# Performance work log

Measured on AMD Instinct MI355X. Metric: run time of the kernel, lower is better.

Reference implementation:

```python
import jax, jax.numpy as jnp
import numpy as np

SEQ, B, XD = 2048, 4, 16
D, NH, DFF, L, M = 256, 8, 512, 2, 1024
DH = D // NH
NEG_INF = -1e9  # finite stand-in for -inf (same softmax result, grad-safe)


def setup_inputs() -> dict:
    key = jax.random.key(0)
    ks = iter(jax.random.split(key, 40))

    def w(shape, s=0.02):
        return jax.random.normal(next(ks), shape, dtype=jnp.float32) * s

    return {
        "x": jax.random.normal(next(ks), (SEQ, B, XD), dtype=jnp.float32),
        "y": jax.random.normal(next(ks), (SEQ, B), dtype=jnp.float32),
        "single_eval_pos": M,
        "xenc_w": w((D, XD)), "xenc_b": w((D,)),
        "yenc_w": w((D, 1)), "yenc_b": w((D,)),
        "in_proj_w": w((L, 3 * D, D)), "in_proj_b": w((L, 3 * D)),
        "out_proj_w": w((L, D, D)), "out_proj_b": w((L, D)),
        "ln1_g": jnp.ones((L, D), jnp.float32), "ln1_b": jnp.zeros((L, D), jnp.float32),
        "lin1_w": w((L, DFF, D)), "lin1_b": w((L, DFF)),
        "lin2_w": w((L, D, DFF)), "lin2_b": w((L, D)),
        "ln2_g": jnp.ones((L, D), jnp.float32), "ln2_b": jnp.zeros((L, D), jnp.float32),
        "head_w1": w((DFF, D)), "head_b1": w((DFF,)),
        "head_w2": w((1, DFF)), "head_b2": w((1,)),
    }


def _layer_norm(x, g, b, eps=1e-5):
    mu = jnp.mean(x, axis=-1, keepdims=True)
    var = jnp.var(x, axis=-1, keepdims=True)
    return (x - mu) * jax.lax.rsqrt(var + eps) * g + b


def _forward(x, y, M_, p):
    seq, batch = y.shape
    x_src = x @ p["xenc_w"].T + p["xenc_b"]                     # [seq, b, D]
    y_src = y[..., None] @ p["yenc_w"].T + p["yenc_b"]           # [seq, b, D]
    tokens = jnp.concatenate([x_src[:M_] + y_src[:M_], x_src[M_:]], axis=0)

    # prefix-block + diagonal mask: keep (j < M) or (i == j)
    i = jnp.arange(seq)
    keep = (i[None, :] < M_) | (i[:, None] == i[None, :])
    mask = jnp.where(keep, 0.0, NEG_INF).astype(tokens.dtype)    # [seq, seq]

    h = tokens
    for l in range(p["in_proj_w"].shape[0]):
        qkv = h @ p["in_proj_w"][l].T + p["in_proj_b"][l]        # [seq, b, 3D]
        q, k, v = jnp.split(qkv, 3, axis=-1)
        to_heads = lambda t: t.reshape(seq, batch, NH, DH).transpose(1, 2, 0, 3)
        q, k, v = to_heads(q), to_heads(k), to_heads(v)          # [b, h, s, dh]
        scores = jnp.einsum("bhqd,bhkd->bhqk", q, k) / np.float32(np.sqrt(DH)) + mask
        attn = jax.nn.softmax(scores, axis=-1)
        o = jnp.einsum("bhqk,bhkd->bhqd", attn, v)
        o = o.transpose(2, 0, 1, 3).reshape(seq, batch, D)
        o = o @ p["out_proj_w"][l].T + p["out_proj_b"][l]
        h = _layer_norm(h + o, p["ln1_g"][l], p["ln1_b"][l])      # post-norm
        ff = jax.nn.gelu(h @ p["lin1_w"][l].T + p["lin1_b"][l], approximate=False)
        ff = ff @ p["lin2_w"][l].T + p["lin2_b"][l]
        h = _layer_norm(h + ff, p["ln2_g"][l], p["ln2_b"][l])

    q_out = h[M_:]                                               # [seq-M, b, D]
    hid = jax.nn.gelu(q_out @ p["head_w1"].T + p["head_b1"], approximate=False)
    return hid @ p["head_w2"].T + p["head_b2"]                   # [seq-M, b, 1]


def reference(x, y, single_eval_pos, xenc_w, xenc_b, yenc_w, yenc_b,
              in_proj_w, in_proj_b, out_proj_w, out_proj_b,
              ln1_g, ln1_b, lin1_w, lin1_b, lin2_w, lin2_b, ln2_g, ln2_b,
              head_w1, head_b1, head_w2, head_b2):
    p = dict(xenc_w=xenc_w, xenc_b=xenc_b, yenc_w=yenc_w, yenc_b=yenc_b,
             in_proj_w=in_proj_w, in_proj_b=in_proj_b,
             out_proj_w=out_proj_w, out_proj_b=out_proj_b,
             ln1_g=ln1_g, ln1_b=ln1_b, lin1_w=lin1_w, lin1_b=lin1_b,
             lin2_w=lin2_w, lin2_b=lin2_b, ln2_g=ln2_g, ln2_b=ln2_b,
             head_w1=head_w1, head_b1=head_b1, head_w2=head_w2, head_b2=head_b2)
    return _forward(x, y, int(single_eval_pos), p)
```

## Files before the change

### kernel.cpp

```cpp
#include <hip/hip_runtime.h>
#include <hip/hip_bf16.h>
#include <math.h>

#define SEQ    2048
#define BATCH  4
#define XDIM   16
#define DMODEL 256
#define NHEAD  8
#define DH     32
#define DFF    512
#define NLAYER 2
#define MPOS   1024
#define ROWS   (SEQ*BATCH)

#define ATT_SCALE 0.17677669529663687f
#define BK 32

typedef __attribute__((ext_vector_type(8))) short bf16x8;
typedef __attribute__((ext_vector_type(4))) float f32x4;

__device__ __forceinline__ float gelu_exact(float x) {
    return 0.5f * x * (1.0f + erff(x * 0.70710678118654752f));
}
__device__ __forceinline__ short f2bf(float f) {
    unsigned int u = __float_as_uint(f);
    u += 0x7FFFu + ((u >> 16) & 1u);
    return (short)(u >> 16);
}
__device__ __forceinline__ float bf2f(unsigned short u) {
    return __uint_as_float(((unsigned int)u) << 16);
}
__device__ __forceinline__ void gload16(const unsigned short* g, unsigned short* l) {
    __builtin_amdgcn_global_load_lds(
        (const __attribute__((address_space(1))) unsigned int*)g,
        (__attribute__((address_space(3))) unsigned int*)l, 16, 0, 0);
}
#define VMWAIT(N) asm volatile("s_waitcnt vmcnt(" #N ")" ::: "memory")
__device__ __forceinline__ void pipe_barrier() {
    __builtin_amdgcn_sched_barrier(0);
    __builtin_amdgcn_s_barrier();
    __builtin_amdgcn_sched_barrier(0);
}

__global__ __launch_bounds__(256) void encode_cast(
    const float* __restrict__ x, const float* __restrict__ y,
    const float* __restrict__ xw, const float* __restrict__ xb,
    const float* __restrict__ yw, const float* __restrict__ yb,
    float* __restrict__ h, unsigned short* __restrict__ hb,
    const float* __restrict__ s0, const float* __restrict__ s1,
    const float* __restrict__ s2, const float* __restrict__ s3,
    const float* __restrict__ s4,
    unsigned short* __restrict__ d0, unsigned short* __restrict__ d1,
    unsigned short* __restrict__ d2, unsigned short* __restrict__ d3,
    unsigned short* __restrict__ d4)
{
    if (blockIdx.x < ROWS/4) {
        int g = blockIdx.x;
        int d = threadIdx.x;
        __shared__ float xs[4][XDIM];
        __shared__ float ys[4];
        if (d < 64) xs[d>>4][d&15] = x[(size_t)(g*4 + (d>>4))*XDIM + (d&15)];
        if (d < 4)  ys[d] = y[g*4 + d];
        __syncthreads();
        float wreg[XDIM];
        #pragma unroll
        for (int k = 0; k < XDIM; ++k) wreg[k] = xw[d*XDIM + k];
        const float xbv = xb[d], ywv = yw[d], ybv = yb[d];
        const bool train = (g < MPOS);
        #pragma unroll
        for (int r = 0; r < 4; ++r) {
            int row = g*4 + r;
            float acc = xbv;
            #pragma unroll
            for (int k = 0; k < XDIM; ++k) acc = fmaf(xs[r][k], wreg[k], acc);
            if (train) acc += ys[r]*ywv + ybv;
            h[(size_t)row*DMODEL + d]  = acc;
            hb[(size_t)row*DMODEL + d] = (unsigned short)f2bf(acc);
        }
        return;
    }
    int i = (blockIdx.x - ROWS/4)*256 + threadIdx.x;
    if (i >= 147456) return;
    const float* s; unsigned short* d; int off;
    if      (i <  49152) { s = s0; d = d0; off = i; }
    else if (i <  65536) { s = s1; d = d1; off = i - 49152; }
    else if (i <  98304) { s = s2; d = d2; off = i - 65536; }
    else if (i < 131072) { s = s3; d = d3; off = i - 98304; }
    else                 { s = s4; d = d4; off = i - 131072; }
    float4 a = *(const float4*)(s + (size_t)off*8);
    float4 c = *(const float4*)(s + (size_t)off*8 + 4);
    ushort4 u0, u1;
    u0.x=(unsigned short)f2bf(a.x); u0.y=(unsigned short)f2bf(a.y);
    u0.z=(unsigned short)f2bf(a.z); u0.w=(unsigned short)f2bf(a.w);
    u1.x=(unsigned short)f2bf(c.x); u1.y=(unsigned short)f2bf(c.y);
    u1.z=(unsigned short)f2bf(c.z); u1.w=(unsigned short)f2bf(c.w);
    *(ushort4*)(d + (size_t)off*8)     = u0;
    *(ushort4*)(d + (size_t)off*8 + 4) = u1;
}

__global__ __launch_bounds__(256) void gemm_qkv(
    const unsigned short* __restrict__ A, const unsigned short* __restrict__ B,
    const float* __restrict__ bias,
    unsigned short* __restrict__ Qg, unsigned short* __restrict__ Kg,
    unsigned short* __restrict__ Vg, int K)
{
    __shared__ unsigned short As[3][128][BK];
    __shared__ unsigned short Bs[3][64][BK];
    int tid  = threadIdx.x;
    int w    = tid >> 6, lane = tid & 63;
    int col  = lane & 15, quad = lane >> 4;
    int u    = blockIdx.x >> 3, xcd = blockIdx.x & 7;
    int by   = xcd*8 + u/12, bx = u%12;
    int m0   = by * 128, n0 = bx * 64;
    int l4   = lane >> 2, c8 = (lane & 3) * 8;

    f32x4 acc[2][4];
    #pragma unroll
    for (int i = 0; i < 2; ++i)
        #pragma unroll
        for (int j = 0; j < 4; ++j) acc[i][j] = (f32x4){0.f,0.f,0.f,0.f};

    const unsigned short* ga = A + (size_t)(m0 + w*32 + l4)*K + c8;
    const unsigned short* gb = B + (size_t)(n0 + w*16 + l4)*K + c8;

    const int NS = K / BK;
    gload16(ga,                  &As[0][w*32     ][0]);
    gload16(ga + (size_t)16*K,   &As[0][w*32 + 16][0]);
    gload16(gb,                  &Bs[0][w*16     ][0]);
    gload16(ga + BK,                  &As[1][w*32     ][0]);
    gload16(ga + BK + (size_t)16*K,   &As[1][w*32 + 16][0]);
    gload16(gb + BK,                  &Bs[1][w*16     ][0]);

    int bcur = 0;
    for (int s = 0; s < NS; ++s) {
        if (s == NS - 1) { VMWAIT(0); } else { VMWAIT(3); }
        pipe_barrier();
        if (s + 2 < NS) {
            int bpre = bcur + 2; if (bpre >= 3) bpre -= 3;
            int k2 = (s + 2) * BK;
            gload16(ga + k2,                &As[bpre][w*32     ][0]);
            gload16(ga + k2 + (size_t)16*K, &As[bpre][w*32 + 16][0]);
            gload16(gb + k2,                &Bs[bpre][w*16     ][0]);
        }
        bf16x8 af[2], bfr[4];
        #pragma unroll
        for (int i = 0; i < 2; ++i) af[i]  = *(const bf16x8*)&As[bcur][w*32 + i*16 + col][quad*8];
        #pragma unroll
        for (int j = 0; j < 4; ++j) bfr[j] = *(const bf16x8*)&Bs[bcur][j*16 + col][quad*8];
        #pragma unroll
        for (int i = 0; i < 2; ++i)
            #pragma unroll
            for (int j = 0; j < 4; ++j)
                acc[i][j] = __builtin_amdgcn_mfma_f32_16x16x32_bf16(bfr[j], af[i], acc[i][j], 0, 0, 0);
        bcur = (bcur == 2) ? 0 : bcur + 1;
    }

    int region = n0 >> 8;
    if (region < 2) {
        #pragma unroll
        for (int i = 0; i < 2; ++i) {
            int m = m0 + w*32 + i*16 + col;
            int s = m >> 2, bidx = m & 3;
            #pragma unroll
            for (int j = 0; j < 4; ++j) {
                int ng = n0 + j*16 + quad*4;
                float4 bi = *(const float4*)&bias[ng];
                ushort4 uu;
                uu.x=(unsigned short)f2bf(acc[i][j][0] + bi.x);
                uu.y=(unsigned short)f2bf(acc[i][j][1] + bi.y);
                uu.z=(unsigned short)f2bf(acc[i][j][2] + bi.z);
                uu.w=(unsigned short)f2bf(acc[i][j][3] + bi.w);
                int np = ng - (region << 8);
                int hh = np >> 5, d = np & 31;
                int bh = bidx*NHEAD + hh;
                if (region == 0)
                    *(ushort4*)(Qg + ((size_t)(bh*SEQ + s))*DH + d) = uu;
                else
                    *(ushort4*)(Kg + ((size_t)(bh*SEQ + s))*DH + d) = uu;
            }
        }
    } else {
        __syncthreads();
        unsigned short* T3 = (unsigned short*)As;
        #pragma unroll
        for (int i = 0; i < 2; ++i) {
            int mi = w*32 + i*16 + col;
            int ss = mi >> 2, bidx = mi & 3;
            #pragma unroll
            for (int j = 0; j < 4; ++j) {
                int ni = j*16 + quad*4;
                float4 bi = *(const float4*)&bias[n0 + ni];
                T3[((ni    )*4 + bidx)*32 + ss] = (unsigned short)f2bf(acc[i][j][0] + bi.x);
                T3[((ni + 1)*4 + bidx)*32 + ss] = (unsigned short)f2bf(acc[i][j][1] + bi.y);
                T3[((ni + 2)*4 + bidx)*32 + ss] = (unsigned short)f2bf(acc[i][j][2] + bi.z);
                T3[((ni + 3)*4 + bidx)*32 + ss] = (unsigned short)f2bf(acc[i][j][3] + bi.w);
            }
        }
        __syncthreads();
        int sBase = m0 >> 2;
        #pragma unroll
        for (int r = 0; r < 4; ++r) {
            int chunk = tid + 256*r;
            int l = chunk >> 2, p = chunk & 3;
            int d = l & 31, hh_l = (l >> 5) & 1, bidx = l >> 6;
            int ni = hh_l*32 + d;
            int hh = ((n0 & 255) + ni) >> 5;
            int bh = bidx*NHEAD + hh;
            uint4 val = *(const uint4*)&T3[(ni*4 + bidx)*32 + p*8];
            *(uint4*)(Vg + ((size_t)(bh*DH + d))*SEQ + sBase + p*8) = val;
        }
    }
}

__global__ __launch_bounds__(256) void attn_mfma(
    const unsigned short* __restrict__ Qg,
    const unsigned short* __restrict__ Kg,
    const unsigned short* __restrict__ Vg,
    unsigned short* __restrict__ o)
{
    const int id  = blockIdx.x;
    const int sl  = id >> 3;
    const int bh  = (id & 7) * 4 + (sl >> 4);
    const int qt2 = sl & 15;
    const int h   = bh & 7;
    const int b   = bh >> 3;
    const int q0A = qt2 * 64;
    const int q0B = MPOS + qt2 * 64;
    const int tid  = threadIdx.x;
    const int w    = tid >> 6;
    const int lane = tid & 63;
    const int col  = lane & 15;
    const int quad = lane >> 4;

    __shared__ unsigned short Kt[2][64][40];
    __shared__ unsigned short Vt[2][32][72];
    __shared__ unsigned short PtA[4][16][72];
    __shared__ unsigned short PtB[4][16][72];

    const int qA = q0A + 16*w + col;
    const int qB = q0B + 16*w + col;
    bf16x8 qfA = *(const bf16x8*)(Qg + ((size_t)(bh*SEQ + qA))*DH + quad*8);
    bf16x8 qfB = *(const bf16x8*)(Qg + ((size_t)(bh*SEQ + qB))*DH + quad*8);

    f32x4 O0A = {0.f,0.f,0.f,0.f}, O1A = {0.f,0.f,0.f,0.f};
    f32x4 O0B = {0.f,0.f,0.f,0.f}, O1B = {0.f,0.f,0.f,0.f};
    float lsumA = 0.f, lsumB = 0.f;

    const int kRow = tid >> 2, kCh = (tid & 3) * 8;
    const int vD   = tid >> 3, vCh = (tid & 7) * 8;

    uint4 kreg = *(const uint4*)(Kg + ((size_t)(bh*SEQ + kRow))*DH + kCh);
    uint4 vreg = *(const uint4*)(Vg + ((size_t)(bh*DH + vD))*SEQ + vCh);

    for (int kt = 0; kt < 17; ++kt) {
        const bool self = (kt == 16);
        const int  p    = kt & 1;
        *(uint4*)&Kt[p][kRow][kCh] = kreg;
        *(uint4*)&Vt[p][vD][vCh]   = vreg;
        __syncthreads();
        if (kt < 16) {
            int kn = (kt == 15) ? q0B : (kt + 1)*64;
            kreg = *(const uint4*)(Kg + ((size_t)(bh*SEQ + kn + kRow))*DH + kCh);
            vreg = *(const uint4*)(Vg + ((size_t)(bh*DH + vD))*SEQ + kn + vCh);
        }

        #pragma unroll
        for (int mt = 0; mt < 4; ++mt) {
            bf16x8 kf = *(const bf16x8*)&Kt[p][mt*16 + col][quad*8];
            if (!self) {
                f32x4 stA = {0.f,0.f,0.f,0.f};
                stA = __builtin_amdgcn_mfma_f32_16x16x32_bf16(kf, qfA, stA, 0, 0, 0);
                ushort4 pwA;
                #pragma unroll
                for (int i = 0; i < 4; ++i) {
                    float pv = __expf(stA[i]*ATT_SCALE);
                    unsigned short us = (unsigned short)f2bf(pv);
                    ((unsigned short*)&pwA)[i] = us;
                    lsumA += bf2f(us);
                }
                *(ushort4*)&PtA[w][col][mt*16 + quad*4] = pwA;
            }
            f32x4 stB = {0.f,0.f,0.f,0.f};
            stB = __builtin_amdgcn_mfma_f32_16x16x32_bf16(kf, qfB, stB, 0, 0, 0);
            ushort4 pwB;
            #pragma unroll
            for (int i = 0; i < 4; ++i) {
                float pv = __expf(stB[i]*ATT_SCALE);
                if (self && (mt*16 + quad*4 + i != 16*w + col)) pv = 0.f;
                unsigned short us = (unsigned short)f2bf(pv);
                ((unsigned short*)&pwB)[i] = us;
                lsumB += bf2f(us);
            }
            *(ushort4*)&PtB[w][col][mt*16 + quad*4] = pwB;
        }
        #pragma unroll
        for (int c = 0; c < 2; ++c) {
            bf16x8 v0 = *(const bf16x8*)&Vt[p][col     ][c*32 + quad*8];
            bf16x8 v1 = *(const bf16x8*)&Vt[p][col + 16][c*32 + quad*8];
            if (!self) {
                bf16x8 pfA = *(const bf16x8*)&PtA[w][col][c*32 + quad*8];
                O0A = __builtin_amdgcn_mfma_f32_16x16x32_bf16(v0, pfA, O0A, 0, 0, 0);
                O1A = __builtin_amdgcn_mfma_f32_16x16x32_bf16(v1, pfA, O1A, 0, 0, 0);
            }
            bf16x8 pfB = *(const bf16x8*)&PtB[w][col][c*32 + quad*8];
            O0B = __builtin_amdgcn_mfma_f32_16x16x32_bf16(v0, pfB, O0B, 0, 0, 0);
            O1B = __builtin_amdgcn_mfma_f32_16x16x32_bf16(v1, pfB, O1B, 0, 0, 0);
        }
    }

    lsumA += __shfl_xor(lsumA, 16, 64); lsumA += __shfl_xor(lsumA, 32, 64);
    lsumB += __shfl_xor(lsumB, 16, 64); lsumB += __shfl_xor(lsumB, 32, 64);
    float invA = 1.0f / lsumA, invB = 1.0f / lsumB;
    ushort4 u0, u1;
    #pragma unroll
    for (int i = 0; i < 4; ++i) {
        ((unsigned short*)&u0)[i] = (unsigned short)f2bf(O0A[i]*invA);
        ((unsigned short*)&u1)[i] = (unsigned short)f2bf(O1A[i]*invA);
    }
    unsigned short* opA = o + ((size_t)(qA*BATCH + b))*DMODEL + h*DH;
    *(ushort4*)(opA + quad*4)      = u0;
    *(ushort4*)(opA + 16 + quad*4) = u1;
    #pragma unroll
    for (int i = 0; i < 4; ++i) {
        ((unsigned short*)&u0)[i] = (unsigned short)f2bf(O0B[i]*invB);
        ((unsigned short*)&u1)[i] = (unsigned short)f2bf(O1B[i]*invB);
    }
    unsigned short* opB = o + ((size_t)(qB*BATCH + b))*DMODEL + h*DH;
    *(ushort4*)(opB + quad*4)      = u0;
    *(ushort4*)(opB + 16 + quad*4) = u1;
}

__global__ __launch_bounds__(256) void mlp_fused(
    const unsigned short* __restrict__ attb,
    const unsigned short* __restrict__ Wout, const float* __restrict__ ob,
    const float* __restrict__ g1, const float* __restrict__ be1,
    const unsigned short* __restrict__ W1, const float* __restrict__ fb1,
    const unsigned short* __restrict__ W2, const float* __restrict__ fb2,
    const float* __restrict__ g2, const float* __restrict__ be2,
    float* __restrict__ h, unsigned short* __restrict__ hb,
    const unsigned short* __restrict__ Wh1, const float* __restrict__ hb1,
    const float* __restrict__ hw2, const float* __restrict__ hb2,
    float* __restrict__ out, int doHead)
{
    __shared__ unsigned short Bs[3][256][64];
    __shared__ __align__(16) unsigned char smem_u[33280];
    __shared__ unsigned short Ht[2][16][264];
    __shared__ float sP[2][4][16], qP[2][4][16];

    typedef unsigned short AsT[2][16][64];
    AsT* As = reinterpret_cast<AsT*>(smem_u);
    typedef unsigned short PtT[16][520];
    PtT* Pt = reinterpret_cast<PtT*>(smem_u);

    const int tid  = threadIdx.x;
    const int w    = tid >> 6;
    const int lane = tid & 63;
    const int col  = lane & 15;
    const int quad = lane >> 4;
    const int l8   = lane >> 3;
    const int c8s  = (((lane & 7) ^ l8) * 8);
    const int bid  = blockIdx.x;
    const int m0a  = bid * 16;
    const int m0b  = 4096 + bid * 16;
    const int ma   = m0a + col;
    const int mb   = m0b + col;

    float resid[2][4][4];

    {
        f32x4 acc[2][4];
        #pragma unroll
        for (int g = 0; g < 2; ++g)
            #pragma unroll
            for (int j = 0; j < 4; ++j) acc[g][j] = (f32x4){0.f,0.f,0.f,0.f};

        const int gr = w >> 1;
        const unsigned short* gaw = attb + (size_t)((gr ? m0b : m0a) + (w&1)*8 + l8)*DMODEL + c8s;
        const unsigned short* gb  = Wout + (size_t)(w*64 + l8)*DMODEL + c8s;
        const int NS = DMODEL / 64;

        #pragma unroll
        for (int pb = 0; pb < 2; ++pb) {
            int k = pb * 64;
            gload16(gaw + k, &As[pb][gr][(w&1)*8][0]);
            #pragma unroll
            for (int t = 0; t < 8; ++t)
                gload16(gb + k + (size_t)(t*8)*DMODEL, &Bs[pb][w*64 + t*8][0]);
        }
        int bcur = 0;
        for (int s = 0; s < NS; ++s) {
            if (s == NS - 1) { VMWAIT(0); } else { VMWAIT(9); }
            pipe_barrier();
            if (s + 2 < NS) {
                int bpre = bcur + 2; if (bpre >= 3) bpre -= 3;
                int k2 = (s + 2) * 64;
                gload16(gaw + k2, &As[bpre][gr][(w&1)*8][0]);
                #pragma unroll
                for (int t = 0; t < 8; ++t)
                    gload16(gb + k2 + (size_t)(t*8)*DMODEL, &Bs[bpre][w*64 + t*8][0]);
            }
            #pragma unroll
            for (int kk = 0; kk < 2; ++kk) {
                const int so = (((kk*4 + quad) ^ (col & 7)) * 8);
                bf16x8 af0 = *(const bf16x8*)&As[bcur][0][col][so];
                bf16x8 af1 = *(const bf16x8*)&As[bcur][1][col][so];
                #pragma unroll
                for (int j = 0; j < 4; ++j) {
                    bf16x8 bfr = *(const bf16x8*)&Bs[bcur][w*64 + j*16 + col][so];
                    acc[0][j] = __builtin_amdgcn_mfma_f32_16x16x32_bf16(bfr, af0, acc[0][j], 0, 0, 0);
                    acc[1][j] = __builtin_amdgcn_mfma_f32_16x16x32_bf16(bfr, af1, acc[1][j], 0, 0, 0);
                }
            }
            bcur = (bcur == 2) ? 0 : bcur + 1;
        }

        float ssum[2] = {0.f, 0.f}, qsum[2] = {0.f, 0.f};
        #pragma unroll
        for (int g = 0; g < 2; ++g) {
            int m = g ? mb : ma;
            #pragma unroll
            for (int j = 0; j < 4; ++j) {
                int n = w*64 + j*16 + quad*4;
                float4 bi = *(const float4*)&ob[n];
                float4 hv = *(const float4*)&h[(size_t)m*DMODEL + n];
                #pragma unroll
                for (int i = 0; i < 4; ++i) {
                    float val = acc[g][j][i] + ((const float*)&bi)[i] + ((const float*)&hv)[i];
                    resid[g][j][i] = val;
                    ssum[g] += val; qsum[g] += val*val;
                }
            }
        }
        #pragma unroll
        for (int g = 0; g < 2; ++g) {
            ssum[g] += __shfl_xor(ssum[g], 16, 64); ssum[g] += __shfl_xor(ssum[g], 32, 64);
            qsum[g] += __shfl_xor(qsum[g], 16, 64); qsum[g] += __shfl_xor(qsum[g], 32, 64);
        }
        if (quad == 0) {
            sP[0][w][col] = ssum[0]; qP[0][w][col] = qsum[0];
            sP[1][w][col] = ssum[1]; qP[1][w][col] = qsum[1];
        }
        __syncthreads();
        #pragma unroll
        for (int g = 0; g < 2; ++g) {
            float st = sP[g][0][col] + sP[g][1][col] + sP[g][2][col] + sP[g][3][col];
            float qt = qP[g][0][col] + qP[g][1][col] + qP[g][2][col] + qP[g][3][col];
            float mu   = st * (1.0f/DMODEL);
            float var  = qt * (1.0f/DMODEL) - mu*mu;
            float rstd = rsqrtf(var + 1e-5f);
            #pragma unroll
            for (int j = 0; j < 4; ++j) {
                int n = w*64 + j*16 + quad*4;
                float4 gv = *(const float4*)&g1[n];
                float4 bv = *(const float4*)&be1[n];
                ushort4 u;
                #pragma unroll
                for (int i = 0; i < 4; ++i) {
                    float o = (resid[g][j][i]-mu)*rstd*((const float*)&gv)[i] + ((const float*)&bv)[i];
                    resid[g][j][i] = o;
                    ((unsigned short*)&u)[i] = (unsigned short)f2bf(o);
                }
                *(ushort4*)&Ht[g][col][n] = u;
            }
        }
        __syncthreads();
    }

    #pragma unroll 1
    for (int nh = 0; nh < 2; ++nh) {
        f32x4 acc[2][4];
        #pragma unroll
        for (int g = 0; g < 2; ++g)
            #pragma unroll
            for (int j = 0; j < 4; ++j) acc[g][j] = (f32x4){0.f,0.f,0.f,0.f};
        const unsigned short* gb = W1 + (size_t)(nh*256 + w*64 + l8)*DMODEL + c8s;
        const int NS = DMODEL / 64;

        #pragma unroll
        for (int pb = 0; pb < 2; ++pb)
            #pragma unroll
            for (int t = 0; t < 8; ++t)
                gload16(gb + pb*64 + (size_t)(t*8)*DMODEL, &Bs[pb][w*64 + t*8][0]);

        int bcur = 0;
        for (int s = 0; s < NS; ++s) {
            if (s == NS - 1) { VMWAIT(0); } else { VMWAIT(8); }
            pipe_barrier();
            if (s + 2 < NS) {
                int bpre = bcur + 2; if (bpre >= 3) bpre -= 3;
                int k2 = (s + 2) * 64;
                #pragma unroll
                for (int t = 0; t < 8; ++t)
                    gload16(gb + k2 + (size_t)(t*8)*DMODEL, &Bs[bpre][w*64 + t*8][0]);
            }
            #pragma unroll
            for (int kk = 0; kk < 2; ++kk) {
                const int so = (((kk*4 + quad) ^ (col & 7)) * 8);
                bf16x8 af0 = *(const bf16x8*)&Ht[0][col][s*64 + kk*32 + quad*8];
                bf16x8 af1 = *(const bf16x8*)&Ht[1][col][s*64 + kk*32 + quad*8];
                #pragma unroll
                for (int j = 0; j < 4; ++j) {
                    bf16x8 bfr = *(const bf16x8*)&Bs[bcur][w*64 + j*16 + col][so];
                    acc[0][j] = __builtin_amdgcn_mfma_f32_16x16x32_bf16(bfr, af0, acc[0][j], 0, 0, 0);
                    acc[1][j] = __builtin_amdgcn_mfma_f32_16x16x32_bf16(bfr, af1, acc[1][j], 0, 0, 0);
                }
            }
            bcur = (bcur == 2) ? 0 : bcur + 1;
        }
        #pragma unroll
        for (int g = 0; g < 2; ++g)
            #pragma unroll
            for (int j = 0; j < 4; ++j) {
                int n2 = nh*256 + w*64 + j*16 + quad*4;
                float4 bi = *(const float4*)&fb1[n2];
                ushort4 u;
                #pragma unroll
                for (int i = 0; i < 4; ++i)
                    ((unsigned short*)&u)[i] = (unsigned short)f2bf(gelu_exact(acc[g][j][i] + ((const float*)&bi)[i]));
                *(ushort4*)&Pt[g][col][n2] = u;
            }
        pipe_barrier();
    }

    {
        __syncthreads();
        f32x4 acc[2][4];
        #pragma unroll
        for (int g = 0; g < 2; ++g)
            #pragma unroll
            for (int j = 0; j < 4; ++j) acc[g][j] = (f32x4){0.f,0.f,0.f,0.f};
        const unsigned short* gb = W2 + (size_t)(w*64 + l8)*DFF + c8s;
        const int NS = DFF / 64;

        #pragma unroll
        for (int pb = 0; pb < 2; ++pb)
            #pragma unroll
            for (int t = 0; t < 8; ++t)
                gload16(gb + pb*64 + (size_t)(t*8)*DFF, &Bs[pb][w*64 + t*8][0]);

        int bcur = 0;
        for (int s = 0; s < NS; ++s) {
            if (s == NS - 1) { VMWAIT(0); } else { VMWAIT(8); }
            pipe_barrier();
            if (s + 2 < NS) {
                int bpre = bcur + 2; if (bpre >= 3) bpre -= 3;
                int k2 = (s + 2) * 64;
                #pragma unroll
                for (int t = 0; t < 8; ++t)
                    gload16(gb + k2 + (size_t)(t*8)*DFF, &Bs[bpre][w*64 + t*8][0]);
            }
            #pragma unroll
            for (int kk = 0; kk < 2; ++kk) {
                const int so = (((kk*4 + quad) ^ (col & 7)) * 8);
                bf16x8 af0 = *(const bf16x8*)&Pt[0][col][s*64 + kk*32 + quad*8];
                bf16x8 af1 = *(const bf16x8*)&Pt[1][col][s*64 + kk*32 + quad*8];
                #pragma unroll
                for (int j = 0; j < 4; ++j) {
                    bf16x8 bfr = *(const bf16x8*)&Bs[bcur][w*64 + j*16 + col][so];
                    acc[0][j] = __builtin_amdgcn_mfma_f32_16x16x32_bf16(bfr, af0, acc[0][j], 0, 0, 0);
                    acc[1][j] = __builtin_amdgcn_mfma_f32_16x16x32_bf16(bfr, af1, acc[1][j], 0, 0, 0);
                }
            }
            bcur = (bcur == 2) ? 0 : bcur + 1;
        }

        float ssum[2] = {0.f, 0.f}, qsum[2] = {0.f, 0.f};
        #pragma unroll
        for (int g = 0; g < 2; ++g)
            #pragma unroll
            for (int j = 0; j < 4; ++j) {
                int n = w*64 + j*16 + quad*4;
                float4 bi = *(const float4*)&fb2[n];
                #pragma unroll
                for (int i = 0; i < 4; ++i) {
                    float val = acc[g][j][i] + ((const float*)&bi)[i] + resid[g][j][i];
                    resid[g][j][i] = val;
                    ssum[g] += val; qsum[g] += val*val;
                }
            }
        #pragma unroll
        for (int g = 0; g < 2; ++g) {
            ssum[g] += __shfl_xor(ssum[g], 16, 64); ssum[g] += __shfl_xor(ssum[g], 32, 64);
            qsum[g] += __shfl_xor(qsum[g], 16, 64); qsum[g] += __shfl_xor(qsum[g], 32, 64);
        }
        if (quad == 0) {
            sP[0][w][col] = ssum[0]; qP[0][w][col] = qsum[0];
            sP[1][w][col] = ssum[1]; qP[1][w][col] = qsum[1];
        }
        __syncthreads();
        #pragma unroll
        for (int g = 0; g < 2; ++g) {
            int m = g ? mb : ma;
            float st = sP[g][0][col] + sP[g][1][col] + sP[g][2][col] + sP[g][3][col];
            float qt = qP[g][0][col] + qP[g][1][col] + qP[g][2][col] + qP[g][3][col];
            float mu   = st * (1.0f/DMODEL);
            float var  = qt * (1.0f/DMODEL) - mu*mu;
            float rstd = rsqrtf(var + 1e-5f);
            #pragma unroll
            for (int j = 0; j < 4; ++j) {
                int n = w*64 + j*16 + quad*4;
                float4 gv = *(const float4*)&g2[n];
                float4 bv = *(const float4*)&be2[n];
                float4 o;
                ushort4 u;
                #pragma unroll
                for (int i = 0; i < 4; ++i) {
                    float ov = (resid[g][j][i]-mu)*rstd*((const float*)&gv)[i] + ((const float*)&bv)[i];
                    ((float*)&o)[i] = ov;
                    ((unsigned short*)&u)[i] = (unsigned short)f2bf(ov);
                }
                *(float4*)&h[(size_t)m*DMODEL + n] = o;
                *(ushort4*)(hb + (size_t)m*DMODEL + n) = u;
                *(ushort4*)&Ht[g][col][n] = u;
            }
        }
        __syncthreads();
    }

    if (doHead) {
        float sdot = 0.f;
        #pragma unroll 1
        for (int nh = 0; nh < 2; ++nh) {
            f32x4 acc[4];
            #pragma unroll
            for (int j = 0; j < 4; ++j) acc[j] = (f32x4){0.f,0.f,0.f,0.f};
            const unsigned short* gb = Wh1 + (size_t)(nh*256 + w*64 + l8)*DMODEL + c8s;
            const int NS = DMODEL / 64;

            #pragma unroll
            for (int pb = 0; pb < 2; ++pb)
                #pragma unroll
                for (int t = 0; t < 8; ++t)
                    gload16(gb + pb*64 + (size_t)(t*8)*DMODEL, &Bs[pb][w*64 + t*8][0]);

            int bcur = 0;
            for (int s = 0; s < NS; ++s) {
                if (s == NS - 1) { VMWAIT(0); } else { VMWAIT(8); }
                pipe_barrier();
                if (s + 2 < NS) {
                    int bpre = bcur + 2; if (bpre >= 3) bpre -= 3;
                    int k2 = (s + 2) * 64;
                    #pragma unroll
                    for (int t = 0; t < 8; ++t)
                        gload16(gb + k2 + (size_t)(t*8)*DMODEL, &Bs[bpre][w*64 + t*8][0]);
                }
                #pragma unroll
                for (int kk = 0; kk < 2; ++kk) {
                    const int so = (((kk*4 + quad) ^ (col & 7)) * 8);
                    bf16x8 af = *(const bf16x8*)&Ht[1][col][s*64 + kk*32 + quad*8];
                    #pragma unroll
                    for (int j = 0; j < 4; ++j) {
                        bf16x8 bfr = *(const bf16x8*)&Bs[bcur][w*64 + j*16 + col][so];
                        acc[j] = __builtin_amdgcn_mfma_f32_16x16x32_bf16(bfr, af, acc[j], 0, 0, 0);
                    }
                }
                bcur = (bcur == 2) ? 0 : bcur + 1;
            }
            #pragma unroll
            for (int j = 0; j < 4; ++j) {
                int n2 = nh*256 + w*64 + j*16 + quad*4;
                float4 b1v = *(const float4*)&hb1[n2];
                float4 w2v = *(const float4*)&hw2[n2];
                #pragma unroll
                for (int i = 0; i < 4; ++i)
                    sdot += gelu_exact(acc[j][i] + ((const float*)&b1v)[i]) * ((const float*)&w2v)[i];
            }
            pipe_barrier();
        }
        sdot += __shfl_xor(sdot, 16, 64); sdot += __shfl_xor(sdot, 32, 64);
        if (quad == 0) sP[0][w][col] = sdot;
        __syncthreads();
        if (tid < 16)
            out[bid*16 + tid] = sP[0][0][tid] + sP[0][1][tid] + sP[0][2][tid] + sP[0][3][tid] + hb2[0];
    }
}

extern "C" void kernel_launch(void* const* d_in, const int* in_sizes, int n_in,
                              void* d_out, int out_size, void* d_ws, size_t ws_size,
                              hipStream_t stream)
{
    const float* x        = (const float*)d_in[0];
    const float* y        = (const float*)d_in[1];
    const float* xenc_w   = (const float*)d_in[3];
    const float* xenc_b   = (const float*)d_in[4];
    const float* yenc_w   = (const float*)d_in[5];
    const float* yenc_b   = (const float*)d_in[6];
    const float* in_proj_w  = (const float*)d_in[7];
    const float* in_proj_b  = (const float*)d_in[8];
    const float* out_proj_w = (const float*)d_in[9];
    const float* out_proj_b = (const float*)d_in[10];
    const float* ln1_g    = (const float*)d_in[11];
    const float* ln1_b    = (const float*)d_in[12];
    const float* lin1_w   = (const float*)d_in[13];
    const float* lin1_b   = (const float*)d_in[14];
    const float* lin2_w   = (const float*)d_in[15];
    const float* lin2_b   = (const float*)d_in[16];
    const float* ln2_g    = (const float*)d_in[17];
    const float* ln2_b    = (const float*)d_in[18];
    const float* head_w1  = (const float*)d_in[19];
    const float* head_b1  = (const float*)d_in[20];
    const float* head_w2  = (const float*)d_in[21];
    const float* head_b2  = (const float*)d_in[22];
    float* out = (float*)d_out;

    float* ws  = (float*)d_ws;
    float* h    = ws;
    unsigned short* hb    = (unsigned short*)(h + (size_t)ROWS*DMODEL);
    unsigned short* attb  = hb    + (size_t)ROWS*DMODEL;
    unsigned short* Qg    = attb  + (size_t)ROWS*DMODEL;
    unsigned short* Kg    = Qg    + (size_t)BATCH*NHEAD*SEQ*DH;
    unsigned short* Vg    = Kg    + (size_t)BATCH*NHEAD*SEQ*DH;
    unsigned short* Wqkv  = Vg    + (size_t)BATCH*NHEAD*SEQ*DH;
    unsigned short* Wout  = Wqkv  + (size_t)NLAYER*3*DMODEL*DMODEL;
    unsigned short* Wl1   = Wout  + (size_t)NLAYER*DMODEL*DMODEL;
    unsigned short* Wl2   = Wl1   + (size_t)NLAYER*DFF*DMODEL;
    unsigned short* Wh1   = Wl2   + (size_t)NLAYER*DMODEL*DFF;

    encode_cast<<<ROWS/4 + 576, 256, 0, stream>>>(
        x, y, xenc_w, xenc_b, yenc_w, yenc_b, h, hb,
        in_proj_w, out_proj_w, lin1_w, lin2_w, head_w1,
        Wqkv, Wout, Wl1, Wl2, Wh1);

    for (int l = 0; l < NLAYER; ++l) {
        gemm_qkv<<<768, 256, 0, stream>>>(
            hb, Wqkv + (size_t)l*3*DMODEL*DMODEL, in_proj_b + l*3*DMODEL,
            Qg, Kg, Vg, DMODEL);
        attn_mfma<<<512, 256, 0, stream>>>(Qg, Kg, Vg, attb);
        mlp_fused<<<256, 256, 0, stream>>>(
            attb,
            Wout + (size_t)l*DMODEL*DMODEL, out_proj_b + l*DMODEL,
            ln1_g + l*DMODEL, ln1_b + l*DMODEL,
            Wl1 + (size_t)l*DFF*DMODEL, lin1_b + l*DFF,
            Wl2 + (size_t)l*DMODEL*DFF, lin2_b + l*DMODEL,
            ln2_g + l*DMODEL, ln2_b + l*DMODEL,
            h, hb,
            Wh1, head_b1, head_w2, head_b2,
            out, (l == NLAYER-1) ? 1 : 0);
    }
}
```

Measured before the change: 249.4 us.

## Widen QKV GEMM K-tile with XOR-swizzled LDS and enlarge attention key tiles

The QKV GEMM moves from a triple-buffered 32-wide K step to a double-buffered 64-wide K step. An XOR swizzle on the LDS column offset is meant to avoid bank conflicts, and the number of barrier and wait steps is halved. The attention kernel now processes 128 keys per iteration instead of 64, with the masked self (diagonal) tile peeled into a separate epilogue. This removes the per-tile `self` branches and halves the sync count. The cost is more LDS and registers per block, which may lower occupancy, and the GEMM now waits on all loads each step with less prefetch depth.

```diff
diff --git a/kernel.cpp b/kernel.cpp
--- a/kernel.cpp
+++ b/kernel.cpp
@@ -14,7 +14,6 @@
 #define ROWS   (SEQ*BATCH)
 
 #define ATT_SCALE 0.17677669529663687f
-#define BK 32
 
 typedef __attribute__((ext_vector_type(8))) short bf16x8;
 typedef __attribute__((ext_vector_type(4))) float f32x4;
@@ -104,15 +103,16 @@
     unsigned short* __restrict__ Qg, unsigned short* __restrict__ Kg,
     unsigned short* __restrict__ Vg, int K)
 {
-    __shared__ unsigned short As[3][128][BK];
-    __shared__ unsigned short Bs[3][64][BK];
+    __shared__ unsigned short As[2][128][64];
+    __shared__ unsigned short Bs[2][64][64];
     int tid  = threadIdx.x;
     int w    = tid >> 6, lane = tid & 63;
     int col  = lane & 15, quad = lane >> 4;
     int u    = blockIdx.x >> 3, xcd = blockIdx.x & 7;
     int by   = xcd*8 + u/12, bx = u%12;
     int m0   = by * 128, n0 = bx * 64;
-    int l4   = lane >> 2, c8 = (lane & 3) * 8;
+    int l8   = lane >> 3;
+    int c8s  = (((lane & 7) ^ l8) * 8);
 
     f32x4 acc[2][4];
     #pragma unroll
@@ -120,39 +120,41 @@
         #pragma unroll
         for (int j = 0; j < 4; ++j) acc[i][j] = (f32x4){0.f,0.f,0.f,0.f};
 
-    const unsigned short* ga = A + (size_t)(m0 + w*32 + l4)*K + c8;
-    const unsigned short* gb = B + (size_t)(n0 + w*16 + l4)*K + c8;
-
-    const int NS = K / BK;
-    gload16(ga,                  &As[0][w*32     ][0]);
-    gload16(ga + (size_t)16*K,   &As[0][w*32 + 16][0]);
-    gload16(gb,                  &Bs[0][w*16     ][0]);
-    gload16(ga + BK,                  &As[1][w*32     ][0]);
-    gload16(ga + BK + (size_t)16*K,   &As[1][w*32 + 16][0]);
-    gload16(gb + BK,                  &Bs[1][w*16     ][0]);
-
-    int bcur = 0;
+    const unsigned short* ga = A + (size_t)(m0 + w*32 + l8)*K + c8s;
+    const unsigned short* gb = B + (size_t)(n0 + w*16 + l8)*K + c8s;
+    const int NS = K / 64;
+
+    #pragma unroll
+    for (int t = 0; t < 4; ++t) gload16(ga + (size_t)(t*8)*K, &As[0][w*32 + t*8][0]);
+    #pragma unroll
+    for (int t = 0; t < 2; ++t) gload16(gb + (size_t)(t*8)*K, &Bs[0][w*16 + t*8][0]);
+
     for (int s = 0; s < NS; ++s) {
-        if (s == NS - 1) { VMWAIT(0); } else { VMWAIT(3); }
+        VMWAIT(0);
         pipe_barrier();
-        if (s + 2 < NS) {
-            int bpre = bcur + 2; if (bpre >= 3) bpre -= 3;
-            int k2 = (s + 2) * BK;
-            gload16(ga + k2,                &As[bpre][w*32     ][0]);
-            gload16(ga + k2 + (size_t)16*K, &As[bpre][w*32 + 16][0]);
-            gload16(gb + k2,                &Bs[bpre][w*16     ][0]);
-        }
-        bf16x8 af[2], bfr[4];
-        #pragma unroll
-        for (int i = 0; i < 2; ++i) af[i]  = *(const bf16x8*)&As[bcur][w*32 + i*16 + col][quad*8];
-        #pragma unroll
-        for (int j = 0; j < 4; ++j) bfr[j] = *(const bf16x8*)&Bs[bcur][j*16 + col][quad*8];
-        #pragma unroll
-        for (int i = 0; i < 2; ++i)
-            #pragma unroll
-            for (int j = 0; j < 4; ++j)
-                acc[i][j] = __builtin_amdgcn_mfma_f32_16x16x32_bf16(bfr[j], af[i], acc[i][j], 0, 0, 0);
-        bcur = (bcur == 2) ? 0 : bcur + 1;
+        if (s + 1 < NS) {
+            int k2 = (s + 1) * 64;
+            int nb = (s + 1) & 1;
+            #pragma unroll
+            for (int t = 0; t < 4; ++t) gload16(ga + k2 + (size_t)(t*8)*K, &As[nb][w*32 + t*8][0]);
+            #pragma unroll
+            for (int t = 0; t < 2; ++t) gload16(gb + k2 + (size_t)(t*8)*K, &Bs[nb][w*16 + t*8][0]);
+        }
+        int cur = s & 1;
+        #pragma unroll
+        for (int kk = 0; kk < 2; ++kk) {
+            const int so = (((kk*4 + quad) ^ (col & 7)) * 8);
+            bf16x8 af[2], bfr[4];
+            #pragma unroll
+            for (int i = 0; i < 2; ++i) af[i]  = *(const bf16x8*)&As[cur][w*32 + i*16 + col][so];
+            #pragma unroll
+            for (int j = 0; j < 4; ++j) bfr[j] = *(const bf16x8*)&Bs[cur][j*16 + col][so];
+            #pragma unroll
+            for (int i = 0; i < 2; ++i)
+                #pragma unroll
+                for (int j = 0; j < 4; ++j)
+                    acc[i][j] = __builtin_amdgcn_mfma_f32_16x16x32_bf16(bfr[j], af[i], acc[i][j], 0, 0, 0);
+        }
     }
 
     int region = n0 >> 8;
@@ -232,10 +234,10 @@
     const int col  = lane & 15;
     const int quad = lane >> 4;
 
-    __shared__ unsigned short Kt[2][64][40];
-    __shared__ unsigned short Vt[2][32][72];
-    __shared__ unsigned short PtA[4][16][72];
-    __shared__ unsigned short PtB[4][16][72];
+    __shared__ unsigned short Kt[2][128][40];
+    __shared__ unsigned short Vt[2][32][136];
+    __shared__ unsigned short PtA[4][16][136];
+    __shared__ unsigned short PtB[4][16][136];
 
     const int qA = q0A + 16*w + col;
     const int qB = q0B + 16*w + col;
@@ -249,44 +251,50 @@
     const int kRow = tid >> 2, kCh = (tid & 3) * 8;
     const int vD   = tid >> 3, vCh = (tid & 7) * 8;
 
-    uint4 kreg = *(const uint4*)(Kg + ((size_t)(bh*SEQ + kRow))*DH + kCh);
-    uint4 vreg = *(const uint4*)(Vg + ((size_t)(bh*DH + vD))*SEQ + vCh);
-
-    for (int kt = 0; kt < 17; ++kt) {
-        const bool self = (kt == 16);
-        const int  p    = kt & 1;
-        *(uint4*)&Kt[p][kRow][kCh] = kreg;
-        *(uint4*)&Vt[p][vD][vCh]   = vreg;
-        __syncthreads();
-        if (kt < 16) {
-            int kn = (kt == 15) ? q0B : (kt + 1)*64;
-            kreg = *(const uint4*)(Kg + ((size_t)(bh*SEQ + kn + kRow))*DH + kCh);
-            vreg = *(const uint4*)(Vg + ((size_t)(bh*DH + vD))*SEQ + kn + vCh);
-        }
-
-        #pragma unroll
-        for (int mt = 0; mt < 4; ++mt) {
+    uint4 kreg0 = *(const uint4*)(Kg + ((size_t)(bh*SEQ + kRow     ))*DH + kCh);
+    uint4 kreg1 = *(const uint4*)(Kg + ((size_t)(bh*SEQ + kRow + 64))*DH + kCh);
+    uint4 vreg0 = *(const uint4*)(Vg + ((size_t)(bh*DH + vD))*SEQ + vCh);
+    uint4 vreg1 = *(const uint4*)(Vg + ((size_t)(bh*DH + vD))*SEQ + vCh + 64);
+
+    for (int kt = 0; kt < 8; ++kt) {
+        const int p = kt & 1;
+        *(uint4*)&Kt[p][kRow     ][kCh] = kreg0;
+        *(uint4*)&Kt[p][kRow + 64][kCh] = kreg1;
+        *(uint4*)&Vt[p][vD][vCh     ]   = vreg0;
+        *(uint4*)&Vt[p][vD][vCh + 64]   = vreg1;
+        __syncthreads();
+        if (kt < 7) {
+            int kn = (kt + 1) * 128;
+            kreg0 = *(const uint4*)(Kg + ((size_t)(bh*SEQ + kn + kRow     ))*DH + kCh);
+            kreg1 = *(const uint4*)(Kg + ((size_t)(bh*SEQ + kn + kRow + 64))*DH + kCh);
+            vreg0 = *(const uint4*)(Vg + ((size_t)(bh*DH + vD))*SEQ + kn + vCh);
+            vreg1 = *(const uint4*)(Vg + ((size_t)(bh*DH + vD))*SEQ + kn + vCh + 64);
+        } else {
+            kreg0 = *(const uint4*)(Kg + ((size_t)(bh*SEQ + q0B + kRow))*DH + kCh);
+            vreg0 = *(const uint4*)(Vg + ((size_t)(bh*DH + vD))*SEQ + q0B + vCh);
+        }
+
+        #pragma unroll
+        for (int mt = 0; mt < 8; ++mt) {
             bf16x8 kf = *(const bf16x8*)&Kt[p][mt*16 + col][quad*8];
-            if (!self) {
-                f32x4 stA = {0.f,0.f,0.f,0.f};
-                stA = __builtin_amdgcn_mfma_f32_16x16x32_bf16(kf, qfA, stA, 0, 0, 0);
-                ushort4 pwA;
-                #pragma unroll
-                for (int i = 0; i < 4; ++i) {
-                    float pv = __expf(stA[i]*ATT_SCALE);
-                    unsigned short us = (unsigned short)f2bf(pv);
-                    ((unsigned short*)&pwA)[i] = us;
-                    lsumA += bf2f(us);
-                }
-                *(ushort4*)&PtA[w][col][mt*16 + quad*4] = pwA;
-            }
+            f32x4 stA = {0.f,0.f,0.f,0.f};
+            stA = __builtin_amdgcn_mfma_f32_16x16x32_bf16(kf, qfA, stA, 0, 0, 0);
+            ushort4 pwA;
+            #pragma unroll
+            for (int i = 0; i < 4; ++i) {
+                float pv = __expf(stA[i]*ATT_SCALE);
+                unsigned short us = (unsigned short)f2bf(pv);
+                ((unsigned short*)&pwA)[i] = us;
+                lsumA += bf2f(us);
+            }
+            *(ushort4*)&PtA[w][col][mt*16 + quad*4] = pwA;
+
             f32x4 stB = {0.f,0.f,0.f,0.f};
             stB = __builtin_amdgcn_mfma_f32_16x16x32_bf16(kf, qfB, stB, 0, 0, 0);
             ushort4 pwB;
             #pragma unroll
             for (int i = 0; i < 4; ++i) {
                 float pv = __expf(stB[i]*ATT_SCALE);
-                if (self && (mt*16 + quad*4 + i != 16*w + col)) pv = 0.f;
                 unsigned short us = (unsigned short)f2bf(pv);
                 ((unsigned short*)&pwB)[i] = us;
                 lsumB += bf2f(us);
@@ -294,18 +302,44 @@
             *(ushort4*)&PtB[w][col][mt*16 + quad*4] = pwB;
         }
         #pragma unroll
-        for (int c = 0; c < 2; ++c) {
+        for (int c = 0; c < 4; ++c) {
             bf16x8 v0 = *(const bf16x8*)&Vt[p][col     ][c*32 + quad*8];
             bf16x8 v1 = *(const bf16x8*)&Vt[p][col + 16][c*32 + quad*8];
-            if (!self) {
-                bf16x8 pfA = *(const bf16x8*)&PtA[w][col][c*32 + quad*8];
-                O0A = __builtin_amdgcn_mfma_f32_16x16x32_bf16(v0, pfA, O0A, 0, 0, 0);
-                O1A = __builtin_amdgcn_mfma_f32_16x16x32_bf16(v1, pfA, O1A, 0, 0, 0);
-            }
+            bf16x8 pfA = *(const bf16x8*)&PtA[w][col][c*32 + quad*8];
+            O0A = __builtin_amdgcn_mfma_f32_16x16x32_bf16(v0, pfA, O0A, 0, 0, 0);
+            O1A = __builtin_amdgcn_mfma_f32_16x16x32_bf16(v1, pfA, O1A, 0, 0, 0);
             bf16x8 pfB = *(const bf16x8*)&PtB[w][col][c*32 + quad*8];
             O0B = __builtin_amdgcn_mfma_f32_16x16x32_bf16(v0, pfB, O0B, 0, 0, 0);
             O1B = __builtin_amdgcn_mfma_f32_16x16x32_bf16(v1, pfB, O1B, 0, 0, 0);
         }
+    }
+
+    *(uint4*)&Kt[0][kRow][kCh] = kreg0;
+    *(uint4*)&Vt[0][vD][vCh]   = vreg0;
+    __syncthreads();
+    #pragma unroll
+    for (int mt = 0; mt < 4; ++mt) {
+        bf16x8 kf = *(const bf16x8*)&Kt[0][mt*16 + col][quad*8];
+        f32x4 stB = {0.f,0.f,0.f,0.f};
+        stB = __builtin_amdgcn_mfma_f32_16x16x32_bf16(kf, qfB, stB, 0, 0, 0);
+        ushort4 pwB;
+        #pragma unroll
+        for (int i = 0; i < 4; ++i) {
+            float pv = __expf(stB[i]*ATT_SCALE);
+            if (mt*16 + quad*4 + i != 16*w + col) pv = 0.f;
+            unsigned short us = (unsigned short)f2bf(pv);
+            ((unsigned short*)&pwB)[i] = us;
+            lsumB += bf2f(us);
+        }
+        *(ushort4*)&PtB[w][col][mt*16 + quad*4] = pwB;
+    }
+    #pragma unroll
+    for (int c = 0; c < 2; ++c) {
+        bf16x8 v0 = *(const bf16x8*)&Vt[0][col     ][c*32 + quad*8];
+        bf16x8 v1 = *(const bf16x8*)&Vt[0][col + 16][c*32 + quad*8];
+        bf16x8 pfB = *(const bf16x8*)&PtB[w][col][c*32 + quad*8];
+        O0B = __builtin_amdgcn_mfma_f32_16x16x32_bf16(v0, pfB, O0B, 0, 0, 0);
+        O1B = __builtin_amdgcn_mfma_f32_16x16x32_bf16(v1, pfB, O1B, 0, 0, 0);
     }
 
     lsumA += __shfl_xor(lsumA, 16, 64); lsumA += __shfl_xor(lsumA, 32, 64);
```

Measured after the change: 236.4 us. 1.05x faster.
